# Kernel tuning notes

Hardware: AMD Instinct MI355X
Metric: run time of the kernel (lower is better)

The kernel has to match this reference:

```python
import jax, jax.numpy as jnp
import numpy as np

NEG_INF = -1e10
LEAK = 0.01


def gatconv(x, adj, w, a_param):
    # x: [B, Cin, N]; w: [Cin, Cout]; a_param: [2*Cout, N]; adj: [N, N]
    C = w.shape[1]
    wh = jnp.einsum('biv,io->bov', x, w)                # [B, Cout, N]
    wh1 = jnp.einsum('biv,io->bov', wh, a_param[:C])    # [B, N, N]
    wh2 = jnp.einsum('biv,io->bov', wh, a_param[C:])    # [B, N, N]
    e = jax.nn.leaky_relu(wh1 + wh2, negative_slope=LEAK)
    att = jnp.where(adj[None] > 1e-6, e, NEG_INF)
    att = jax.nn.softmax(att, axis=1)                   # softmax over source nodes (dim 1)
    h = jnp.einsum('bin,bov->bon', att, wh)             # [B, Cout, N]
    return jax.nn.elu(h)                                # GATConv concat=True -> elu


def gat_mh(x, adj, w1, a1, w2, a2):
    # head=1, support_len=1; dropout is identity in eval mode.
    h = jax.nn.elu(gatconv(x, adj, w1, a1))   # inner GAT wrapper elu
    h = jax.nn.elu(gatconv(h, adj, w2, a2))   # out_att GAT wrapper elu
    return jax.nn.elu(h)                      # GAT_MH final elu


def setup_inputs() -> dict:
    key = jax.random.key(0)
    ks = jax.random.split(key, 10)
    B, C, N, T = 8, 32, 512, 12
    inp = jax.random.normal(ks[0], (B, C, N, T), dtype=jnp.float32)
    cell = jax.random.normal(ks[1], (B, C, N, 1), dtype=jnp.float32)
    u = jax.random.uniform(ks[2], (N, N), dtype=jnp.float32)
    adj = jnp.maximum(jnp.where(u < 0.06, 1.0, 0.0), jnp.eye(N, dtype=jnp.float32))
    # 12 timesteps x 8 GAT_MH modules, each = 2 GATConvs (inner head + out_att)
    w1 = jax.random.normal(ks[3], (T, 8, C, C), dtype=jnp.float32) * 0.05
    a1 = jax.random.normal(ks[4], (T, 8, 2 * C, N), dtype=jnp.float32) * 0.05
    w2 = jax.random.normal(ks[5], (T, 8, C, C), dtype=jnp.float32) * 0.05
    a2 = jax.random.normal(ks[6], (T, 8, 2 * C, N), dtype=jnp.float32) * 0.05
    # i/f/o/c biases, each [C, N, T]
    bias = (jax.random.uniform(ks[7], (4, C, N, T), dtype=jnp.float32) - 0.5) * (2.0 / np.sqrt(N))
    return {'input': inp, 'cell': cell, 'adj': adj, 'w1': w1, 'a1': a1, 'w2': w2, 'a2': a2, 'bias': bias}


def reference(input, cell, adj, w1, a1, w2, a2, bias):
    B, C, N, T = input.shape
    c0 = cell[..., 0]                       # [B, C, N]
    xs_t = jnp.moveaxis(input, -1, 0)       # [T, B, C, N]
    bias_t = jnp.moveaxis(bias, -1, 0)      # [T, 4, C, N]

    def step(c, xs):
        x_t, w1t, a1t, w2t, a2t, bt = xs
        stacked = jnp.concatenate([
            jnp.broadcast_to(x_t[None], (4, B, C, N)),
            jnp.broadcast_to(c[None], (4, B, C, N)),
        ], axis=0)                          # [8, B, C, N]
        outs = jax.vmap(gat_mh, in_axes=(0, None, 0, 0, 0, 0))(stacked, adj, w1t, a1t, w2t, a2t)
        g = outs[:4] + bt[:, None]          # gates from x_t, plus per-gate bias
        s = outs[4:]                        # gates from cell
        i = jax.nn.sigmoid(g[0] + s[0])
        f = jax.nn.sigmoid(g[1] + s[1])
        o = jax.nn.sigmoid(g[2] + s[2])
        ct = jnp.tanh(g[3] + s[3])
        c_new = f * c + i * ct
        H = o * jnp.tanh(c_new)
        return c_new, H

    c_final, Hs = jax.lax.scan(step, c0, (xs_t, w1, a1, w2, a2, bias_t))
    output = jnp.moveaxis(Hs, 0, -1)        # [B, C, N, T]
    return output, c_final[..., None]
```

## Files before the change

### kernel.cpp

```cpp
#include <hip/hip_runtime.h>

typedef unsigned long long u64;

#define CC 32
#define NN 512
#define TT 12
#define NBLK 256
#define NTHR 256

__device__ __forceinline__ float eluf(float x){ return x>0.f ? x : (__expf(x)-1.f); }
__device__ __forceinline__ float elu3f(float x){ return eluf(eluf(eluf(x))); }
__device__ __forceinline__ float sigmf(float x){
  if (x>=0.f) return 1.f/(1.f+__expf(-x));
  float e=__expf(x); return e/(1.f+e);
}
__device__ __forceinline__ float tanhff(float x){
  return 1.f - 2.f/(__expf(2.f*x)+1.f);
}
__device__ __forceinline__ u64 pack_slot(unsigned tag, float v){
  return ((u64)tag<<32) | (u64)__float_as_uint(v);
}
__device__ __forceinline__ u64 ld_slot(u64* p){
  return __hip_atomic_load(p, __ATOMIC_RELAXED, __HIP_MEMORY_SCOPE_AGENT);
}
__device__ __forceinline__ void xch_slot(u64* p, u64 v){
  (void)__hip_atomic_exchange(p, v, __ATOMIC_RELAXED, __HIP_MEMORY_SCOPE_AGENT);
}
__device__ __forceinline__ float poll_slot(u64* p, unsigned want){
  u64 v = ld_slot(p);
  int guard = 0;
  while ((unsigned)(v>>32) != want){
    __builtin_amdgcn_s_sleep(1);
    v = ld_slot(p);
    if (++guard > 1000000) break;
  }
  return __uint_as_float((unsigned)v);
}

__global__ __launch_bounds__(NTHR, 1)
void glstm_fused(const float* __restrict__ xg,
                 const float* __restrict__ cellg,
                 const float* __restrict__ w1g,
                 const float* __restrict__ w2g,
                 const float* __restrict__ biasg,
                 float* __restrict__ outg,
                 u64* slots)
{
  __shared__ float biasL[4][TT][NN];
  __shared__ float preS[2][4];
  __shared__ float redS[2][4];
  __shared__ float wpart[13][4];

  const int blk  = blockIdx.x;
  const int b    = blk >> 5;
  const int ch   = blk & 31;
  const int row  = blk;
  const int tid  = threadIdx.x;
  const int lane = tid & 63;
  const int wv   = tid >> 6;
  const int i0   = lane & 31;

  u64* cs_slot = slots;
  u64* xs_slot = slots + 2*NBLK;

  const int n0 = 2*tid;
  float2 cc2 = *(const float2*)(cellg + row*NN + n0);
  float c0 = cc2.x, c1 = cc2.y;

  float xs[TT];
  #pragma unroll
  for (int t=0;t<TT;t++) xs[t]=0.f;
  const float* xrow = xg + row*NN*TT;
  #pragma unroll
  for (int half=0; half<2; half++){
    int n = tid + half*256;
    const float4* p = (const float4*)(xrow + n*TT);
    float4 v0=p[0], v1=p[1], v2=p[2];
    xs[0]+=v0.x;  xs[1]+=v0.y;  xs[2]+=v0.z;  xs[3]+=v0.w;
    xs[4]+=v1.x;  xs[5]+=v1.y;  xs[6]+=v1.z;  xs[7]+=v1.w;
    xs[8]+=v2.x;  xs[9]+=v2.y;  xs[10]+=v2.z; xs[11]+=v2.w;
  }
  float cp = c0 + c1;
  #pragma unroll
  for (int off=32; off>=1; off>>=1){
    #pragma unroll
    for (int t=0;t<TT;t++) xs[t] += __shfl_xor(xs[t], off, 64);
    cp += __shfl_xor(cp, off, 64);
  }
  if (lane == 0){
    #pragma unroll
    for (int t=0;t<TT;t++) wpart[t][wv] = xs[t];
    wpart[12][wv] = cp;
  }
  __syncthreads();
  if (tid < 13){
    float v = wpart[tid][0]+wpart[tid][1]+wpart[tid][2]+wpart[tid][3];
    if (tid < TT) xch_slot(&xs_slot[tid*NBLK + row], pack_slot(1u, v));
    else          xch_slot(&cs_slot[row],            pack_slot(1u, v));
  }

  #pragma unroll
  for (int k=0;k<4;k++){
    #pragma unroll
    for (int half=0; half<2; half++){
      int n = tid + half*256;
      const float4* p = (const float4*)(biasg + ((k*CC + ch)*NN + n)*TT);
      float4 v0=p[0], v1=p[1], v2=p[2];
      biasL[k][0][n]=v0.x;  biasL[k][1][n]=v0.y;  biasL[k][2][n]=v0.z;  biasL[k][3][n]=v0.w;
      biasL[k][4][n]=v1.x;  biasL[k][5][n]=v1.y;  biasL[k][6][n]=v1.z;  biasL[k][7][n]=v1.w;
      biasL[k][8][n]=v2.x;  biasL[k][9][n]=v2.y;  biasL[k][10][n]=v2.z; biasL[k][11][n]=v2.w;
    }
  }

  const int m = wv + ((lane >> 5) << 2);
  float w1p[2][32];
  float w2p[2];
  {
    const float* w1m = w1g + m*CC*CC + i0;
    #pragma unroll
    for (int j=0;j<32;j++) w1p[0][j] = w1m[j*CC];
    w2p[0] = w2g[(m*CC + i0)*CC + ch];
  }

  float zxr[TT];
  #pragma unroll
  for (int t=0;t<TT;t++)
    zxr[t] = poll_slot(&xs_slot[t*NBLK + b*CC + i0], 1u);

  float hm0[TT], hm1[TT];
  #pragma unroll
  for (int s=0;s<TT;s++){
    float csv = poll_slot(&cs_slot[(s&1)*NBLK + b*CC + i0], (unsigned)(s+1));
    float zs = (lane < 32) ? zxr[s] : csv;

    float pa = 0.f, pb = 0.f;
    #pragma unroll
    for (int j=0;j<16;j++){
      pa = fmaf(__shfl(zs, j,    32), w1p[s&1][j],    pa);
      pb = fmaf(__shfl(zs, j+16, 32), w1p[s&1][j+16], pb);
    }
    float s1 = pa + pb;
    float h1 = eluf(eluf(s1));
    float pp = h1 * w2p[s&1];
    #pragma unroll
    for (int off=16; off>=1; off>>=1) pp += __shfl_xor(pp, off, 32);
    float ov = elu3f(512.f*pp);
    float prew = ov + __shfl_xor(ov, 32, 64);
    if (lane == 0) preS[s&1][wv] = prew;

    float b00 = biasL[0][s][n0], b01 = biasL[0][s][n0+1];
    float b10 = biasL[1][s][n0], b11 = biasL[1][s][n0+1];
    float b20 = biasL[2][s][n0], b21 = biasL[2][s][n0+1];
    float b30 = biasL[3][s][n0], b31 = biasL[3][s][n0+1];

    __syncthreads();
    const float g0 = preS[s&1][0], g1 = preS[s&1][1];
    const float g2 = preS[s&1][2], g3 = preS[s&1][3];

    float ig0 = sigmf(g0 + b00);
    float fg0 = sigmf(g1 + b10);
    float ct0 = tanhff(g3 + b30);
    float ig1 = sigmf(g0 + b01);
    float fg1 = sigmf(g1 + b11);
    float ct1 = tanhff(g3 + b31);
    c0 = fg0*c0 + ig0*ct0;
    c1 = fg1*c1 + ig1*ct1;

    if (s < TT-1){
      const int par = (s+1)&1;
      float csp = c0 + c1;
      #pragma unroll
      for (int off=32; off>=1; off>>=1) csp += __shfl_xor(csp, off, 64);
      if (lane == 0) redS[par][wv] = csp;
      __syncthreads();
      if (tid == 0){
        float tot = redS[par][0]+redS[par][1]+redS[par][2]+redS[par][3];
        xch_slot(&cs_slot[par*NBLK + row], pack_slot((unsigned)(s+2), tot));
      }
      const float* w1m = w1g + ((s+1)*8 + m)*CC*CC + i0;
      #pragma unroll
      for (int j=0;j<32;j++) w1p[par][j] = w1m[j*CC];
      w2p[par] = w2g[(((s+1)*8 + m)*CC + i0)*CC + ch];
    }

    hm0[s] = sigmf(g2 + b20) * tanhff(c0);
    hm1[s] = sigmf(g2 + b21) * tanhff(c1);
  }

  float4* op = (float4*)(outg + (row*NN + n0)*TT);
  op[0] = make_float4(hm0[0], hm0[1], hm0[2],  hm0[3]);
  op[1] = make_float4(hm0[4], hm0[5], hm0[6],  hm0[7]);
  op[2] = make_float4(hm0[8], hm0[9], hm0[10], hm0[11]);
  op[3] = make_float4(hm1[0], hm1[1], hm1[2],  hm1[3]);
  op[4] = make_float4(hm1[4], hm1[5], hm1[6],  hm1[7]);
  op[5] = make_float4(hm1[8], hm1[9], hm1[10], hm1[11]);
  *(float2*)(outg + NBLK*NN*TT + row*NN + n0) = make_float2(c0, c1);
}

extern "C" void kernel_launch(void* const* d_in, const int* in_sizes, int n_in,
                              void* d_out, int out_size, void* d_ws, size_t ws_size,
                              hipStream_t stream)
{
  (void)in_sizes; (void)n_in; (void)out_size; (void)ws_size;
  const float* xg    = (const float*)d_in[0];
  const float* cellg = (const float*)d_in[1];
  const float* w1g   = (const float*)d_in[3];
  const float* w2g   = (const float*)d_in[5];
  const float* biasg = (const float*)d_in[7];
  float* outg = (float*)d_out;
  u64* slots = (u64*)d_ws;

  hipMemsetAsync(d_ws, 0, (size_t)(2*NBLK + TT*NBLK)*sizeof(u64), stream);
  glstm_fused<<<dim3(NBLK), dim3(NTHR), 0, stream>>>(xg, cellg, w1g, w2g, biasg, outg, slots);
}
```

Before: 43.53 us.

## Merge four channels per block to shrink cross-block sync and drop LDS bias staging

Each block now handles four channels with 512 threads across 64 blocks, down from one channel per block across 256 blocks. This cuts the number of participants in the global-memory slot handshake, and each warp now computes all four w2 projections for its module. Bias is kept in registers and reloaded every four steps instead of staged in LDS. Outputs are written directly each step. A large dummy shared array is added, probably to control occupancy and block placement. The trade-off is more per-block serial work and per-step uncoalesced stores in exchange for fewer spinning blocks.

```diff
diff --git a/kernel.cpp b/kernel.cpp
--- a/kernel.cpp
+++ b/kernel.cpp
@@ -5,8 +5,10 @@
 #define CC 32
 #define NN 512
 #define TT 12
-#define NBLK 256
-#define NTHR 256
+#define BB 8
+#define CHPB 4
+#define NBLK 64
+#define NTHR 512
 
 __device__ __forceinline__ float eluf(float x){ return x>0.f ? x : (__expf(x)-1.f); }
 __device__ __forceinline__ float elu3f(float x){ return eluf(eluf(eluf(x))); }
@@ -36,8 +38,11 @@
   }
   return __uint_as_float((unsigned)v);
 }
-
-__global__ __launch_bounds__(NTHR, 1)
+__device__ __forceinline__ float fcomp(float4 v, int c){
+  return c==0 ? v.x : c==1 ? v.y : c==2 ? v.z : v.w;
+}
+
+__global__ __launch_bounds__(NTHR, 2)
 void glstm_fused(const float* __restrict__ xg,
                  const float* __restrict__ cellg,
                  const float* __restrict__ w1g,
@@ -46,41 +51,44 @@
                  float* __restrict__ outg,
                  u64* slots)
 {
-  __shared__ float biasL[4][TT][NN];
-  __shared__ float preS[2][4];
-  __shared__ float redS[2][4];
-  __shared__ float wpart[13][4];
+  __shared__ float pad[21504];
+  __shared__ float outL[8][CHPB];
+  __shared__ float redL[8];
+  __shared__ float xpartL[TT][8];
+  __shared__ float cpartL[8];
 
   const int blk  = blockIdx.x;
-  const int b    = blk >> 5;
-  const int ch   = blk & 31;
-  const int row  = blk;
+  const int b    = blk >> 3;
+  const int ch0  = (blk & 7) * CHPB;
   const int tid  = threadIdx.x;
   const int lane = tid & 63;
   const int wv   = tid >> 6;
   const int i0   = lane & 31;
+  const int chl  = tid >> 7;
+  const int ch   = ch0 + chl;
+  const int nbase= (tid & 127) * 4;
+  const int rowc = b*CC + ch;
 
   u64* cs_slot = slots;
-  u64* xs_slot = slots + 2*NBLK;
-
-  const int n0 = 2*tid;
-  float2 cc2 = *(const float2*)(cellg + row*NN + n0);
-  float c0 = cc2.x, c1 = cc2.y;
+  u64* xs_slot = slots + 2*256;
+
+  if (tid == 0) ((volatile float*)pad)[0] = 0.f;
+
+  float4 cv = *(const float4*)(cellg + rowc*NN + nbase);
+  float c0=cv.x, c1=cv.y, c2=cv.z, c3=cv.w;
 
   float xs[TT];
   #pragma unroll
   for (int t=0;t<TT;t++) xs[t]=0.f;
-  const float* xrow = xg + row*NN*TT;
-  #pragma unroll
-  for (int half=0; half<2; half++){
-    int n = tid + half*256;
-    const float4* p = (const float4*)(xrow + n*TT);
-    float4 v0=p[0], v1=p[1], v2=p[2];
-    xs[0]+=v0.x;  xs[1]+=v0.y;  xs[2]+=v0.z;  xs[3]+=v0.w;
-    xs[4]+=v1.x;  xs[5]+=v1.y;  xs[6]+=v1.z;  xs[7]+=v1.w;
-    xs[8]+=v2.x;  xs[9]+=v2.y;  xs[10]+=v2.z; xs[11]+=v2.w;
-  }
-  float cp = c0 + c1;
+  const float4* xp = (const float4*)(xg + (rowc*NN + nbase)*TT);
+  #pragma unroll
+  for (int nl=0; nl<4; nl++){
+    float4 a=xp[nl*3+0], d=xp[nl*3+1], e=xp[nl*3+2];
+    xs[0]+=a.x; xs[1]+=a.y; xs[2]+=a.z;  xs[3]+=a.w;
+    xs[4]+=d.x; xs[5]+=d.y; xs[6]+=d.z;  xs[7]+=d.w;
+    xs[8]+=e.x; xs[9]+=e.y; xs[10]+=e.z; xs[11]+=e.w;
+  }
+  float cp = c0+c1+c2+c3;
   #pragma unroll
   for (int off=32; off>=1; off>>=1){
     #pragma unroll
@@ -89,112 +97,125 @@
   }
   if (lane == 0){
     #pragma unroll
-    for (int t=0;t<TT;t++) wpart[t][wv] = xs[t];
-    wpart[12][wv] = cp;
+    for (int t=0;t<TT;t++) xpartL[t][wv] = xs[t];
+    cpartL[wv] = cp;
   }
   __syncthreads();
-  if (tid < 13){
-    float v = wpart[tid][0]+wpart[tid][1]+wpart[tid][2]+wpart[tid][3];
-    if (tid < TT) xch_slot(&xs_slot[tid*NBLK + row], pack_slot(1u, v));
-    else          xch_slot(&cs_slot[row],            pack_slot(1u, v));
-  }
-
-  #pragma unroll
-  for (int k=0;k<4;k++){
-    #pragma unroll
-    for (int half=0; half<2; half++){
-      int n = tid + half*256;
-      const float4* p = (const float4*)(biasg + ((k*CC + ch)*NN + n)*TT);
-      float4 v0=p[0], v1=p[1], v2=p[2];
-      biasL[k][0][n]=v0.x;  biasL[k][1][n]=v0.y;  biasL[k][2][n]=v0.z;  biasL[k][3][n]=v0.w;
-      biasL[k][4][n]=v1.x;  biasL[k][5][n]=v1.y;  biasL[k][6][n]=v1.z;  biasL[k][7][n]=v1.w;
-      biasL[k][8][n]=v2.x;  biasL[k][9][n]=v2.y;  biasL[k][10][n]=v2.z; biasL[k][11][n]=v2.w;
-    }
-  }
-
-  const int m = wv + ((lane >> 5) << 2);
-  float w1p[2][32];
-  float w2p[2];
+  if (tid < 48){
+    int t = tid>>2, cl = tid&3;
+    float v = xpartL[t][2*cl] + xpartL[t][2*cl+1];
+    xch_slot(&xs_slot[t*256 + b*CC + ch0 + cl], pack_slot(1u, v));
+  } else if (tid < 52){
+    int cl = tid - 48;
+    float v = cpartL[2*cl] + cpartL[2*cl+1];
+    xch_slot(&cs_slot[b*CC + ch0 + cl], pack_slot(1u, v));
+  }
+
+  float4 bch[4][4];
+  #pragma unroll
+  for (int k=0;k<4;k++)
+    #pragma unroll
+    for (int nl=0;nl<4;nl++)
+      bch[k][nl] = *(const float4*)&biasg[((k*CC+ch)*NN + nbase+nl)*TT + 0];
+
+  const int mh = (wv<4) ? (wv+4) : (wv-4);
+  float  w1p[2][32];
+  float4 w2c[2];
   {
-    const float* w1m = w1g + m*CC*CC + i0;
+    const float* w1m = w1g + mh*CC*CC + i0;
     #pragma unroll
     for (int j=0;j<32;j++) w1p[0][j] = w1m[j*CC];
-    w2p[0] = w2g[(m*CC + i0)*CC + ch];
+    w2c[0] = *(const float4*)&w2g[(mh*CC + i0)*CC + ch0];
   }
 
   float zxr[TT];
-  #pragma unroll
-  for (int t=0;t<TT;t++)
-    zxr[t] = poll_slot(&xs_slot[t*NBLK + b*CC + i0], 1u);
-
-  float hm0[TT], hm1[TT];
+  if (wv >= 4){
+    #pragma unroll
+    for (int t=0;t<TT;t++)
+      zxr[t] = poll_slot(&xs_slot[t*256 + b*CC + i0], 1u);
+  }
+
+  float* houtp = outg + (rowc*NN + nbase)*TT;
+
   #pragma unroll
   for (int s=0;s<TT;s++){
-    float csv = poll_slot(&cs_slot[(s&1)*NBLK + b*CC + i0], (unsigned)(s+1));
-    float zs = (lane < 32) ? zxr[s] : csv;
-
-    float pa = 0.f, pb = 0.f;
-    #pragma unroll
-    for (int j=0;j<16;j++){
-      pa = fmaf(__shfl(zs, j,    32), w1p[s&1][j],    pa);
-      pb = fmaf(__shfl(zs, j+16, 32), w1p[s&1][j+16], pb);
-    }
-    float s1 = pa + pb;
-    float h1 = eluf(eluf(s1));
-    float pp = h1 * w2p[s&1];
-    #pragma unroll
-    for (int off=16; off>=1; off>>=1) pp += __shfl_xor(pp, off, 32);
-    float ov = elu3f(512.f*pp);
-    float prew = ov + __shfl_xor(ov, 32, 64);
-    if (lane == 0) preS[s&1][wv] = prew;
-
-    float b00 = biasL[0][s][n0], b01 = biasL[0][s][n0+1];
-    float b10 = biasL[1][s][n0], b11 = biasL[1][s][n0+1];
-    float b20 = biasL[2][s][n0], b21 = biasL[2][s][n0+1];
-    float b30 = biasL[3][s][n0], b31 = biasL[3][s][n0+1];
-
+    {
+      float zs;
+      if (wv < 4) zs = poll_slot(&cs_slot[(s&1)*256 + b*CC + i0], (unsigned)(s+1));
+      else        zs = zxr[s];
+      float s1 = 0.f;
+      #pragma unroll
+      for (int j=0;j<32;j++) s1 = fmaf(__shfl(zs, j, 32), w1p[s&1][j], s1);
+      float h1 = eluf(eluf(s1));
+      float o[4];
+      #pragma unroll
+      for (int cl=0; cl<4; cl++){
+        float pp = h1 * fcomp(w2c[s&1], cl);
+        #pragma unroll
+        for (int off=16; off>=1; off>>=1) pp += __shfl_xor(pp, off, 32);
+        o[cl] = elu3f(512.f*pp);
+      }
+      if (lane == 0){
+        outL[mh][0]=o[0]; outL[mh][1]=o[1]; outL[mh][2]=o[2]; outL[mh][3]=o[3];
+      }
+    }
     __syncthreads();
-    const float g0 = preS[s&1][0], g1 = preS[s&1][1];
-    const float g2 = preS[s&1][2], g3 = preS[s&1][3];
-
-    float ig0 = sigmf(g0 + b00);
-    float fg0 = sigmf(g1 + b10);
-    float ct0 = tanhff(g3 + b30);
-    float ig1 = sigmf(g0 + b01);
-    float fg1 = sigmf(g1 + b11);
-    float ct1 = tanhff(g3 + b31);
-    c0 = fg0*c0 + ig0*ct0;
-    c1 = fg1*c1 + ig1*ct1;
+    const float g0 = outL[0][chl] + outL[4][chl];
+    const float g1 = outL[1][chl] + outL[5][chl];
+    const float g2 = outL[2][chl] + outL[6][chl];
+    const float g3 = outL[3][chl] + outL[7][chl];
+
+    {
+      float ig,fg,ct;
+      ig = sigmf(g0 + fcomp(bch[0][0], s&3));
+      fg = sigmf(g1 + fcomp(bch[1][0], s&3));
+      ct = tanhff(g3 + fcomp(bch[3][0], s&3));
+      c0 = fg*c0 + ig*ct;
+      ig = sigmf(g0 + fcomp(bch[0][1], s&3));
+      fg = sigmf(g1 + fcomp(bch[1][1], s&3));
+      ct = tanhff(g3 + fcomp(bch[3][1], s&3));
+      c1 = fg*c1 + ig*ct;
+      ig = sigmf(g0 + fcomp(bch[0][2], s&3));
+      fg = sigmf(g1 + fcomp(bch[1][2], s&3));
+      ct = tanhff(g3 + fcomp(bch[3][2], s&3));
+      c2 = fg*c2 + ig*ct;
+      ig = sigmf(g0 + fcomp(bch[0][3], s&3));
+      fg = sigmf(g1 + fcomp(bch[1][3], s&3));
+      ct = tanhff(g3 + fcomp(bch[3][3], s&3));
+      c3 = fg*c3 + ig*ct;
+    }
+    float csp = c0+c1+c2+c3;
+    #pragma unroll
+    for (int off=32; off>=1; off>>=1) csp += __shfl_xor(csp, off, 64);
+    if (lane == 0) redL[wv] = csp;
+    __syncthreads();
+    if (s < TT-1 && tid < 4){
+      float tot = redL[2*tid] + redL[2*tid+1];
+      xch_slot(&cs_slot[((s+1)&1)*256 + b*CC + ch0 + tid],
+               pack_slot((unsigned)(s+2), tot));
+    }
+
+    houtp[0*TT + s] = sigmf(g2 + fcomp(bch[2][0], s&3)) * tanhff(c0);
+    houtp[1*TT + s] = sigmf(g2 + fcomp(bch[2][1], s&3)) * tanhff(c1);
+    houtp[2*TT + s] = sigmf(g2 + fcomp(bch[2][2], s&3)) * tanhff(c2);
+    houtp[3*TT + s] = sigmf(g2 + fcomp(bch[2][3], s&3)) * tanhff(c3);
 
     if (s < TT-1){
-      const int par = (s+1)&1;
-      float csp = c0 + c1;
-      #pragma unroll
-      for (int off=32; off>=1; off>>=1) csp += __shfl_xor(csp, off, 64);
-      if (lane == 0) redS[par][wv] = csp;
-      __syncthreads();
-      if (tid == 0){
-        float tot = redS[par][0]+redS[par][1]+redS[par][2]+redS[par][3];
-        xch_slot(&cs_slot[par*NBLK + row], pack_slot((unsigned)(s+2), tot));
-      }
-      const float* w1m = w1g + ((s+1)*8 + m)*CC*CC + i0;
-      #pragma unroll
-      for (int j=0;j<32;j++) w1p[par][j] = w1m[j*CC];
-      w2p[par] = w2g[(((s+1)*8 + m)*CC + i0)*CC + ch];
-    }
-
-    hm0[s] = sigmf(g2 + b20) * tanhff(c0);
-    hm1[s] = sigmf(g2 + b21) * tanhff(c1);
-  }
-
-  float4* op = (float4*)(outg + (row*NN + n0)*TT);
-  op[0] = make_float4(hm0[0], hm0[1], hm0[2],  hm0[3]);
-  op[1] = make_float4(hm0[4], hm0[5], hm0[6],  hm0[7]);
-  op[2] = make_float4(hm0[8], hm0[9], hm0[10], hm0[11]);
-  op[3] = make_float4(hm1[0], hm1[1], hm1[2],  hm1[3]);
-  op[4] = make_float4(hm1[4], hm1[5], hm1[6],  hm1[7]);
-  op[5] = make_float4(hm1[8], hm1[9], hm1[10], hm1[11]);
-  *(float2*)(outg + NBLK*NN*TT + row*NN + n0) = make_float2(c0, c1);
+      const float* w1m = w1g + ((s+1)*8 + mh)*CC*CC + i0;
+      #pragma unroll
+      for (int j=0;j<32;j++) w1p[(s+1)&1][j] = w1m[j*CC];
+      w2c[(s+1)&1] = *(const float4*)&w2g[(((s+1)*8 + mh)*CC + i0)*CC + ch0];
+    }
+    if ((s&3)==3 && s < TT-1){
+      #pragma unroll
+      for (int k=0;k<4;k++)
+        #pragma unroll
+        for (int nl=0;nl<4;nl++)
+          bch[k][nl] = *(const float4*)&biasg[((k*CC+ch)*NN + nbase+nl)*TT + (s+1)];
+    }
+  }
+
+  *(float4*)(outg + BB*CC*NN*TT + rowc*NN + nbase) = make_float4(c0,c1,c2,c3);
 }
 
 extern "C" void kernel_launch(void* const* d_in, const int* in_sizes, int n_in,
@@ -210,6 +231,6 @@
   float* outg = (float*)d_out;
   u64* slots = (u64*)d_ws;
 
-  hipMemsetAsync(d_ws, 0, (size_t)(2*NBLK + TT*NBLK)*sizeof(u64), stream);
+  hipMemsetAsync(d_ws, 0, (size_t)(2*256 + TT*256)*sizeof(u64), stream);
   glstm_fused<<<dim3(NBLK), dim3(NTHR), 0, stream>>>(xg, cellg, w1g, w2g, biasg, outg, slots);
 }
```

New measurement: 77.77 us. 1.79x slower.

## Replace cross-block slot sync with per-batch blocks plus separate bias and output kernels

Applied to the files above, without the earlier changes.

Adds a three-kernel path that runs when workspace is large enough. A bias transpose kernel comes first. Then one 1024-thread block per batch runs the recurrence with block-level syncs instead of inter-block atomic slot polling, and a final kernel computes H from the stored cell history. The aim is to remove global spin-wait synchronisation across 256 blocks. In exchange, only 8 CUs run the serial recurrence, extra kernel launches are added, and the cell history makes a round trip through global memory. The original fused kernel is kept as a fallback.

```diff
diff --git a/kernel.cpp b/kernel.cpp
--- a/kernel.cpp
+++ b/kernel.cpp
@@ -5,8 +5,9 @@
 #define CC 32
 #define NN 512
 #define TT 12
-#define NBLK 256
-#define NTHR 256
+#define BB 8
+#define QTOT (4*CC*NN)
+#define NELEM (BB*CC*NN)
 
 __device__ __forceinline__ float eluf(float x){ return x>0.f ? x : (__expf(x)-1.f); }
 __device__ __forceinline__ float elu3f(float x){ return eluf(eluf(eluf(x))); }
@@ -17,6 +18,181 @@
 __device__ __forceinline__ float tanhff(float x){
   return 1.f - 2.f/(__expf(2.f*x)+1.f);
 }
+
+__global__ __launch_bounds__(256, 4)
+void k_transpose_bias(const float* __restrict__ bg, float* __restrict__ tb){
+  int q = blockIdx.x*256 + threadIdx.x;
+  const float4* p = (const float4*)(bg + q*12);
+  float4 a = p[0], d = p[1], e = p[2];
+  tb[ 0*QTOT + q] = a.x;  tb[ 1*QTOT + q] = a.y;
+  tb[ 2*QTOT + q] = a.z;  tb[ 3*QTOT + q] = a.w;
+  tb[ 4*QTOT + q] = d.x;  tb[ 5*QTOT + q] = d.y;
+  tb[ 6*QTOT + q] = d.z;  tb[ 7*QTOT + q] = d.w;
+  tb[ 8*QTOT + q] = e.x;  tb[ 9*QTOT + q] = e.y;
+  tb[10*QTOT + q] = e.z;  tb[11*QTOT + q] = e.w;
+}
+
+__global__ __launch_bounds__(1024, 1)
+void k_glstm_batch(const float* __restrict__ xg,
+                   const float* __restrict__ cellg,
+                   const float* __restrict__ w1g,
+                   const float* __restrict__ w2g,
+                   const float* __restrict__ tb,
+                   float* __restrict__ chist,
+                   float* __restrict__ g2h,
+                   float* __restrict__ outg)
+{
+  __shared__ float w1L[8][CC][CC];
+  __shared__ float w2L[8][CC][CC];
+  __shared__ float xsumL[TT][CC];
+  __shared__ float csumL[CC];
+  __shared__ float outLh[8][CC];
+
+  const int b    = blockIdx.x;
+  const int t    = threadIdx.x;
+  const int ch   = t >> 5;
+  const int nsub = t & 31;
+  const int nb   = nsub << 4;
+  const int wv   = t >> 6;
+  const int grow = (b*CC + ch)*NN + nb;
+
+  const float4* cp4 = (const float4*)(cellg + grow);
+  float4 c0 = cp4[0], c1 = cp4[1], c2 = cp4[2], c3 = cp4[3];
+
+  float xs[TT];
+  #pragma unroll
+  for (int k=0;k<TT;k++) xs[k]=0.f;
+  const float4* xp = (const float4*)(xg + grow*TT);
+  #pragma unroll
+  for (int j=0;j<16;j++){
+    float4 a=xp[j*3+0], d=xp[j*3+1], e=xp[j*3+2];
+    xs[0]+=a.x; xs[1]+=a.y; xs[2]+=a.z;  xs[3]+=a.w;
+    xs[4]+=d.x; xs[5]+=d.y; xs[6]+=d.z;  xs[7]+=d.w;
+    xs[8]+=e.x; xs[9]+=e.y; xs[10]+=e.z; xs[11]+=e.w;
+  }
+  float cs0 = (c0.x+c0.y+c0.z+c0.w)+(c1.x+c1.y+c1.z+c1.w)
+            + (c2.x+c2.y+c2.z+c2.w)+(c3.x+c3.y+c3.z+c3.w);
+  #pragma unroll
+  for (int off=16; off>=1; off>>=1){
+    #pragma unroll
+    for (int k=0;k<TT;k++) xs[k] += __shfl_xor(xs[k], off, 32);
+    cs0 += __shfl_xor(cs0, off, 32);
+  }
+  if (nsub == 0){
+    #pragma unroll
+    for (int k=0;k<TT;k++) xsumL[k][ch] = xs[k];
+    csumL[ch] = cs0;
+  }
+
+  {
+    const float4* p1 = (const float4*)(w1g);
+    const float4* p2 = (const float4*)(w2g);
+    float4* d1 = (float4*)&w1L[0][0][0];
+    float4* d2 = (float4*)&w2L[0][0][0];
+    d1[t] = p1[t]; d1[t+1024] = p1[t+1024];
+    d2[t] = p2[t]; d2[t+1024] = p2[t+1024];
+  }
+  __syncthreads();
+
+  for (int s=0; s<TT; ++s){
+    if (wv < 4){
+      const int m  = t >> 5;
+      const int ii = t & 31;
+      const float* zrow = (m < 4) ? &xsumL[s][0] : &csumL[0];
+      const float* w1c = &w1L[m][0][ii];
+      float s1 = 0.f;
+      #pragma unroll
+      for (int j=0;j<32;j++) s1 = fmaf(zrow[j], w1c[j*CC], s1);
+      float h1 = eluf(eluf(s1));
+      const float* w2c = &w2L[m][0][ii];
+      float pp = 0.f;
+      #pragma unroll
+      for (int j=0;j<32;j++) pp = fmaf(__shfl(h1, j, 32), w2c[j*CC], pp);
+      outLh[m][ii] = elu3f(512.f*pp);
+    }
+    __syncthreads();
+
+    const float g0 = outLh[0][ch] + outLh[4][ch];
+    const float g1 = outLh[1][ch] + outLh[5][ch];
+    const float g2 = outLh[2][ch] + outLh[6][ch];
+    const float g3 = outLh[3][ch] + outLh[7][ch];
+
+    float4 w1a, w1b, w2a, w2b;
+    if (s < TT-1){
+      const float4* p1 = (const float4*)(w1g + (s+1)*8*CC*CC);
+      const float4* p2 = (const float4*)(w2g + (s+1)*8*CC*CC);
+      w1a = p1[t]; w1b = p1[t+1024];
+      w2a = p2[t]; w2b = p2[t+1024];
+    }
+
+    const float* tbs = tb + s*QTOT;
+    float csp = 0.f;
+    float* chp = chist + s*NELEM + grow;
+    #pragma unroll
+    for (int q=0;q<4;q++){
+      float4 b0v = *(const float4*)(tbs + (0*CC+ch)*NN + nb + q*4);
+      float4 b1v = *(const float4*)(tbs + (1*CC+ch)*NN + nb + q*4);
+      float4 b3v = *(const float4*)(tbs + (3*CC+ch)*NN + nb + q*4);
+      float4* cq = (q==0)?&c0:(q==1)?&c1:(q==2)?&c2:&c3;
+      float ig,fg,ct;
+      ig = sigmf(g0 + b0v.x); fg = sigmf(g1 + b1v.x); ct = tanhff(g3 + b3v.x);
+      cq->x = fg*cq->x + ig*ct;
+      ig = sigmf(g0 + b0v.y); fg = sigmf(g1 + b1v.y); ct = tanhff(g3 + b3v.y);
+      cq->y = fg*cq->y + ig*ct;
+      ig = sigmf(g0 + b0v.z); fg = sigmf(g1 + b1v.z); ct = tanhff(g3 + b3v.z);
+      cq->z = fg*cq->z + ig*ct;
+      ig = sigmf(g0 + b0v.w); fg = sigmf(g1 + b1v.w); ct = tanhff(g3 + b3v.w);
+      cq->w = fg*cq->w + ig*ct;
+      ((float4*)chp)[q] = *cq;
+      csp += cq->x + cq->y + cq->z + cq->w;
+    }
+
+    #pragma unroll
+    for (int off=16; off>=1; off>>=1) csp += __shfl_xor(csp, off, 32);
+    if (nsub == 0){
+      csumL[ch] = csp;
+      g2h[s*BB*CC + b*CC + ch] = g2;
+    }
+
+    if (s < TT-1){
+      float4* d1 = (float4*)&w1L[0][0][0];
+      float4* d2 = (float4*)&w2L[0][0][0];
+      d1[t] = w1a; d1[t+1024] = w1b;
+      d2[t] = w2a; d2[t+1024] = w2b;
+    }
+    __syncthreads();
+  }
+
+  float4* cf = (float4*)(outg + BB*CC*NN*TT + grow);
+  cf[0]=c0; cf[1]=c1; cf[2]=c2; cf[3]=c3;
+}
+
+__global__ __launch_bounds__(256, 4)
+void k_hfinal(const float* __restrict__ chist,
+              const float* __restrict__ tb,
+              const float* __restrict__ g2h,
+              float* __restrict__ outg)
+{
+  int gid = blockIdx.x*256 + threadIdx.x;
+  int bch = gid >> 9;
+  int ch  = bch & 31;
+  int n   = gid & 511;
+  float hm[TT];
+  #pragma unroll
+  for (int s=0;s<TT;s++){
+    float c  = chist[s*NELEM + gid];
+    float b2 = tb[s*QTOT + (2*CC+ch)*NN + n];
+    float g2 = g2h[s*BB*CC + bch];
+    hm[s] = sigmf(g2 + b2) * tanhff(c);
+  }
+  float4* op = (float4*)(outg + gid*TT);
+  op[0] = make_float4(hm[0], hm[1], hm[2],  hm[3]);
+  op[1] = make_float4(hm[4], hm[5], hm[6],  hm[7]);
+  op[2] = make_float4(hm[8], hm[9], hm[10], hm[11]);
+}
+
+#define NBLK8 256
+#define NTHR8 256
 __device__ __forceinline__ u64 pack_slot(unsigned tag, float v){
   return ((u64)tag<<32) | (u64)__float_as_uint(v);
 }
@@ -37,14 +213,11 @@
   return __uint_as_float((unsigned)v);
 }
 
-__global__ __launch_bounds__(NTHR, 1)
-void glstm_fused(const float* __restrict__ xg,
-                 const float* __restrict__ cellg,
-                 const float* __restrict__ w1g,
-                 const float* __restrict__ w2g,
-                 const float* __restrict__ biasg,
-                 float* __restrict__ outg,
-                 u64* slots)
+__global__ __launch_bounds__(NTHR8, 1)
+void glstm_fused_r8(const float* __restrict__ xg, const float* __restrict__ cellg,
+                    const float* __restrict__ w1g, const float* __restrict__ w2g,
+                    const float* __restrict__ biasg, float* __restrict__ outg,
+                    u64* slots)
 {
   __shared__ float biasL[4][TT][NN];
   __shared__ float preS[2][4];
@@ -52,7 +225,7 @@
   __shared__ float wpart[13][4];
 
   const int blk  = blockIdx.x;
-  const int b    = blk >> 5;
+  const int bb   = blk >> 5;
   const int ch   = blk & 31;
   const int row  = blk;
   const int tid  = threadIdx.x;
@@ -61,7 +234,7 @@
   const int i0   = lane & 31;
 
   u64* cs_slot = slots;
-  u64* xs_slot = slots + 2*NBLK;
+  u64* xs_slot = slots + 2*NBLK8;
 
   const int n0 = 2*tid;
   float2 cc2 = *(const float2*)(cellg + row*NN + n0);
@@ -69,7 +242,7 @@
 
   float xs[TT];
   #pragma unroll
-  for (int t=0;t<TT;t++) xs[t]=0.f;
+  for (int k=0;k<TT;k++) xs[k]=0.f;
   const float* xrow = xg + row*NN*TT;
   #pragma unroll
   for (int half=0; half<2; half++){
@@ -84,21 +257,20 @@
   #pragma unroll
   for (int off=32; off>=1; off>>=1){
     #pragma unroll
-    for (int t=0;t<TT;t++) xs[t] += __shfl_xor(xs[t], off, 64);
+    for (int k=0;k<TT;k++) xs[k] += __shfl_xor(xs[k], off, 64);
     cp += __shfl_xor(cp, off, 64);
   }
   if (lane == 0){
     #pragma unroll
-    for (int t=0;t<TT;t++) wpart[t][wv] = xs[t];
+    for (int k=0;k<TT;k++) wpart[k][wv] = xs[k];
     wpart[12][wv] = cp;
   }
   __syncthreads();
   if (tid < 13){
     float v = wpart[tid][0]+wpart[tid][1]+wpart[tid][2]+wpart[tid][3];
-    if (tid < TT) xch_slot(&xs_slot[tid*NBLK + row], pack_slot(1u, v));
-    else          xch_slot(&cs_slot[row],            pack_slot(1u, v));
-  }
-
+    if (tid < TT) xch_slot(&xs_slot[tid*NBLK8 + row], pack_slot(1u, v));
+    else          xch_slot(&cs_slot[row],             pack_slot(1u, v));
+  }
   #pragma unroll
   for (int k=0;k<4;k++){
     #pragma unroll
@@ -111,7 +283,6 @@
       biasL[k][8][n]=v2.x;  biasL[k][9][n]=v2.y;  biasL[k][10][n]=v2.z; biasL[k][11][n]=v2.w;
     }
   }
-
   const int m = wv + ((lane >> 5) << 2);
   float w1p[2][32];
   float w2p[2];
@@ -121,18 +292,16 @@
     for (int j=0;j<32;j++) w1p[0][j] = w1m[j*CC];
     w2p[0] = w2g[(m*CC + i0)*CC + ch];
   }
-
   float zxr[TT];
   #pragma unroll
-  for (int t=0;t<TT;t++)
-    zxr[t] = poll_slot(&xs_slot[t*NBLK + b*CC + i0], 1u);
+  for (int k=0;k<TT;k++)
+    zxr[k] = poll_slot(&xs_slot[k*NBLK8 + bb*CC + i0], 1u);
 
   float hm0[TT], hm1[TT];
   #pragma unroll
   for (int s=0;s<TT;s++){
-    float csv = poll_slot(&cs_slot[(s&1)*NBLK + b*CC + i0], (unsigned)(s+1));
+    float csv = poll_slot(&cs_slot[(s&1)*NBLK8 + bb*CC + i0], (unsigned)(s+1));
     float zs = (lane < 32) ? zxr[s] : csv;
-
     float pa = 0.f, pb = 0.f;
     #pragma unroll
     for (int j=0;j<16;j++){
@@ -175,18 +344,16 @@
       __syncthreads();
       if (tid == 0){
         float tot = redS[par][0]+redS[par][1]+redS[par][2]+redS[par][3];
-        xch_slot(&cs_slot[par*NBLK + row], pack_slot((unsigned)(s+2), tot));
+        xch_slot(&cs_slot[par*NBLK8 + row], pack_slot((unsigned)(s+2), tot));
       }
       const float* w1m = w1g + ((s+1)*8 + m)*CC*CC + i0;
       #pragma unroll
       for (int j=0;j<32;j++) w1p[par][j] = w1m[j*CC];
       w2p[par] = w2g[(((s+1)*8 + m)*CC + i0)*CC + ch];
     }
-
     hm0[s] = sigmf(g2 + b20) * tanhff(c0);
     hm1[s] = sigmf(g2 + b21) * tanhff(c1);
   }
-
   float4* op = (float4*)(outg + (row*NN + n0)*TT);
   op[0] = make_float4(hm0[0], hm0[1], hm0[2],  hm0[3]);
   op[1] = make_float4(hm0[4], hm0[5], hm0[6],  hm0[7]);
@@ -194,22 +361,38 @@
   op[3] = make_float4(hm1[0], hm1[1], hm1[2],  hm1[3]);
   op[4] = make_float4(hm1[4], hm1[5], hm1[6],  hm1[7]);
   op[5] = make_float4(hm1[8], hm1[9], hm1[10], hm1[11]);
-  *(float2*)(outg + NBLK*NN*TT + row*NN + n0) = make_float2(c0, c1);
+  *(float2*)(outg + NBLK8*NN*TT + row*NN + n0) = make_float2(c0, c1);
 }
 
 extern "C" void kernel_launch(void* const* d_in, const int* in_sizes, int n_in,
                               void* d_out, int out_size, void* d_ws, size_t ws_size,
                               hipStream_t stream)
 {
-  (void)in_sizes; (void)n_in; (void)out_size; (void)ws_size;
+  (void)in_sizes; (void)n_in; (void)out_size;
   const float* xg    = (const float*)d_in[0];
   const float* cellg = (const float*)d_in[1];
   const float* w1g   = (const float*)d_in[3];
   const float* w2g   = (const float*)d_in[5];
   const float* biasg = (const float*)d_in[7];
   float* outg = (float*)d_out;
-  u64* slots = (u64*)d_ws;
-
-  hipMemsetAsync(d_ws, 0, (size_t)(2*NBLK + TT*NBLK)*sizeof(u64), stream);
-  glstm_fused<<<dim3(NBLK), dim3(NTHR), 0, stream>>>(xg, cellg, w1g, w2g, biasg, outg, slots);
-}
+
+  const size_t tb_f    = (size_t)TT*QTOT;
+  const size_t chist_f = (size_t)TT*NELEM;
+  const size_t g2_f    = (size_t)TT*BB*CC;
+  const size_t need    = (tb_f + chist_f + g2_f)*sizeof(float);
+
+  if (ws_size >= need){
+    float* tb    = (float*)d_ws;
+    float* chist = tb + tb_f;
+    float* g2h   = chist + chist_f;
+    k_transpose_bias<<<dim3(QTOT/256), dim3(256), 0, stream>>>(biasg, tb);
+    k_glstm_batch<<<dim3(BB), dim3(1024), 0, stream>>>(xg, cellg, w1g, w2g,
+                                                       tb, chist, g2h, outg);
+    k_hfinal<<<dim3(NELEM/256), dim3(256), 0, stream>>>(chist, tb, g2h, outg);
+  } else {
+    u64* slots = (u64*)d_ws;
+    hipMemsetAsync(d_ws, 0, (size_t)(2*NBLK8 + TT*NBLK8)*sizeof(u64), stream);
+    glstm_fused_r8<<<dim3(NBLK8), dim3(NTHR8), 0, stream>>>(xg, cellg, w1g, w2g,
+                                                            biasg, outg, slots);
+  }
+}
```

Measured after the change: 156.5 us. +259.4%, slower.

## Add fast L2-local flag path for cell-sum exchange and remap blocks by batch

Applied to the files above, without the earlier changes.

Block indices are remapped so consecutive blocks belong to different batches, with each batch's 32 channel blocks spread across blocks that step by 8. The per-step cell-sum exchange also gets a second flag array written with plain stores and polled with sc0 loads, with a periodic fallback to the original atomic slot. The aim is to cut inter-block handoff latency on the serial per-timestep dependency, presumably by keeping a batch's blocks on the same XCD L2 so a cheaper non-atomic load can see the update. If the placement assumption fails, correctness relies on the slower fallback poll. It also adds extra stores per step and a race-prone zero init of the fast flags at kernel start.

```diff
diff --git a/kernel.cpp b/kernel.cpp
--- a/kernel.cpp
+++ b/kernel.cpp
@@ -33,6 +33,31 @@
     __builtin_amdgcn_s_sleep(1);
     v = ld_slot(p);
     if (++guard > 1000000) break;
+  }
+  return __uint_as_float((unsigned)v);
+}
+__device__ __forceinline__ u64 l2_load(const u64* p){
+  u64 v;
+  asm volatile("global_load_dwordx2 %0, %1, off sc0\n\t"
+               "s_waitcnt vmcnt(0)"
+               : "=v"(v) : "v"(p) : "memory");
+  return v;
+}
+__device__ __forceinline__ void l2_store(u64* p, u64 v){
+  asm volatile("global_store_dwordx2 %0, %1, off"
+               :: "v"(p), "v"(v) : "memory");
+}
+__device__ __forceinline__ float poll_dual(const u64* fp, u64* sp, unsigned want){
+  u64 v; int it = 0;
+  for (;;){
+    v = l2_load(fp);
+    if ((unsigned)(v>>32) == want) break;
+    if ((it & 15) == 15){
+      v = ld_slot(sp);
+      if ((unsigned)(v>>32) == want) break;
+    }
+    __builtin_amdgcn_s_sleep(1);
+    if (++it > 1000000) break;
   }
   return __uint_as_float((unsigned)v);
 }
@@ -52,16 +77,23 @@
   __shared__ float wpart[13][4];
 
   const int blk  = blockIdx.x;
-  const int b    = blk >> 5;
-  const int ch   = blk & 31;
-  const int row  = blk;
+  const int b    = blk & 7;
+  const int ch   = blk >> 3;
+  const int row  = b*CC + ch;
   const int tid  = threadIdx.x;
   const int lane = tid & 63;
   const int wv   = tid >> 6;
   const int i0   = lane & 31;
 
-  u64* cs_slot = slots;
-  u64* xs_slot = slots + 2*NBLK;
+  u64* scs = slots;
+  u64* sxs = slots + 2*NBLK;
+  u64* fcs = slots + 14*NBLK;
+
+  if (tid == 0){
+    l2_store(&fcs[row], 0);
+    l2_store(&fcs[NBLK + row], 0);
+    asm volatile("s_waitcnt vmcnt(0)" ::: "memory");
+  }
 
   const int n0 = 2*tid;
   float2 cc2 = *(const float2*)(cellg + row*NN + n0);
@@ -95,8 +127,12 @@
   __syncthreads();
   if (tid < 13){
     float v = wpart[tid][0]+wpart[tid][1]+wpart[tid][2]+wpart[tid][3];
-    if (tid < TT) xch_slot(&xs_slot[tid*NBLK + row], pack_slot(1u, v));
-    else          xch_slot(&cs_slot[row],            pack_slot(1u, v));
+    if (tid < TT){
+      xch_slot(&sxs[tid*NBLK + row], pack_slot(1u, v));
+    } else {
+      l2_store(&fcs[row], pack_slot(1u, v));
+      xch_slot(&scs[row], pack_slot(1u, v));
+    }
   }
 
   #pragma unroll
@@ -125,12 +161,15 @@
   float zxr[TT];
   #pragma unroll
   for (int t=0;t<TT;t++)
-    zxr[t] = poll_slot(&xs_slot[t*NBLK + b*CC + i0], 1u);
+    zxr[t] = poll_slot(&sxs[t*NBLK + b*CC + i0], 1u);
 
   float hm0[TT], hm1[TT];
   #pragma unroll
   for (int s=0;s<TT;s++){
-    float csv = poll_slot(&cs_slot[(s&1)*NBLK + b*CC + i0], (unsigned)(s+1));
+    float csv;
+    if (s == 0) csv = poll_slot(&scs[b*CC + i0], 1u);
+    else        csv = poll_dual(&fcs[(s&1)*NBLK + b*CC + i0],
+                                &scs[(s&1)*NBLK + b*CC + i0], (unsigned)(s+1));
     float zs = (lane < 32) ? zxr[s] : csv;
 
     float pa = 0.f, pb = 0.f;
@@ -175,7 +214,9 @@
       __syncthreads();
       if (tid == 0){
         float tot = redS[par][0]+redS[par][1]+redS[par][2]+redS[par][3];
-        xch_slot(&cs_slot[par*NBLK + row], pack_slot((unsigned)(s+2), tot));
+        u64 pk = pack_slot((unsigned)(s+2), tot);
+        l2_store(&fcs[par*NBLK + row], pk);
+        xch_slot(&scs[par*NBLK + row], pk);
       }
       const float* w1m = w1g + ((s+1)*8 + m)*CC*CC + i0;
       #pragma unroll
@@ -210,6 +251,6 @@
   float* outg = (float*)d_out;
   u64* slots = (u64*)d_ws;
 
-  hipMemsetAsync(d_ws, 0, (size_t)(2*NBLK + TT*NBLK)*sizeof(u64), stream);
+  hipMemsetAsync(d_ws, 0, (size_t)(14*NBLK)*sizeof(u64), stream);
   glstm_fused<<<dim3(NBLK), dim3(NTHR), 0, stream>>>(xg, cellg, w1g, w2g, biasg, outg, slots);
 }
```

New measurement: 46.29 us. 1.06x slower.
